# Kernel tuning notes

Measured on AMD Instinct MI355X. Metric: run time of the kernel, lower is better.

Reference implementation:

```python
import jax, jax.numpy as jnp
import numpy as np

B, N, D, H = 4, 512, 4, 256


def _linear_params(key, fan_in, fan_out):
    # torch.nn.Linear default init: U(-1/sqrt(fan_in), 1/sqrt(fan_in))
    lim = 1.0 / np.sqrt(fan_in)
    kw, kb = jax.random.split(key)
    W = jax.random.uniform(kw, (fan_in, fan_out), minval=-lim, maxval=lim, dtype=jnp.float32)
    b = jax.random.uniform(kb, (fan_out,), minval=-lim, maxval=lim, dtype=jnp.float32)
    return W, b


def setup_inputs() -> dict:
    key = jax.random.key(0)
    ks = jax.random.split(key, 8)
    x = jax.random.normal(ks[0], (B, N, D), dtype=jnp.float32)
    adj = jax.random.uniform(ks[1], (B, N, N), dtype=jnp.float32)  # soft adjacency in [0,1)
    W_e1, b_e1 = _linear_params(ks[2], 2 * D, H)
    W_e2, b_e2 = _linear_params(ks[3], H, H)
    W_n1, b_n1 = _linear_params(ks[4], H, H)
    W_n2, b_n2 = _linear_params(ks[5], H, H)
    W_o1, b_o1 = _linear_params(ks[6], D + H, H)
    W_o, b_o = _linear_params(ks[7], H, D)
    return {
        "x": x, "adj": adj,
        "W_e1": W_e1, "b_e1": b_e1, "W_e2": W_e2, "b_e2": b_e2,
        "W_n1": W_n1, "b_n1": b_n1, "W_n2": W_n2, "b_n2": b_n2,
        "W_o1": W_o1, "b_o1": b_o1, "W_o": W_o, "b_o": b_o,
    }


def reference(x, adj, W_e1, b_e1, W_e2, b_e2, W_n1, b_n1, W_n2, b_n2, W_o1, b_o1, W_o, b_o):
    b_, n_, d_ = x.shape
    # innode[b,i,j,:] = x[b,j]; outnode[b,i,j,:] = x[b,i]
    innode = jnp.broadcast_to(x[:, None, :, :], (b_, n_, n_, d_))
    outnode = jnp.broadcast_to(x[:, :, None, :], (b_, n_, n_, d_))
    edge_in = jnp.concatenate([innode, outnode], axis=-1)          # [B,N,N,2D]
    node2edge = jax.nn.relu(edge_in @ W_e1 + b_e1)                 # [B,N,N,H]
    edge2edge = jax.nn.relu(node2edge @ W_e2 + b_e2)               # [B,N,N,H]
    # adjacency-masked sum over axis 1 (the i axis)
    agg = jnp.einsum('bij,bijh->bjh', adj, edge2edge)              # [B,N,H]
    out1 = jax.nn.relu(agg @ W_n1 + b_n1)
    out2 = jax.nn.relu(out1 @ W_n2 + b_n2)
    out3 = jnp.concatenate([x, out2], axis=-1)                     # [B,N,D+H]
    out4 = out3 @ W_o1 + b_o1
    out5 = out4 @ W_o + b_o                                        # [B,N,D]
    # CONTINUOUS is False for the classifier variant
    return jax.nn.log_softmax(out5, axis=2)
```

## Files before the change

### kernel.cpp

```cpp
#include <hip/hip_runtime.h>
#include <hip/hip_fp16.h>
#include <math.h>

#define Bq 4
#define Nq 512
#define Dq 4
#define Hq 256

typedef _Float16 f16x8 __attribute__((ext_vector_type(8)));
typedef float f32x4 __attribute__((ext_vector_type(4)));

__device__ __forceinline__ f16x8 hadd_relu(f16x8 u, f16x8 v) {
    f16x8 s = u + v;
    const f16x8 z = (f16x8)(_Float16)0.0f;
    return __builtin_elementwise_max(s, z);
}

__device__ __forceinline__ uint4 cvt8h(const float* p) {
    union { __half h[8]; uint4 u; } r;
#pragma unroll
    for (int i = 0; i < 8; ++i) r.h[i] = __float2half(p[i]);
    return r.u;
}

__global__ __launch_bounds__(256) void prep_all(
    const float* __restrict__ x, const float* __restrict__ We1,
    const float* __restrict__ be1, __half* __restrict__ U, __half* __restrict__ V,
    const float* __restrict__ Wn1, const float* __restrict__ Wn2,
    const float* __restrict__ Wo1, __half* __restrict__ Wt16) {
    const int bid = blockIdx.x;
    const int t = threadIdx.x;
    if (bid < 256) {
        const float w0 = We1[0 * 256 + t], w1 = We1[1 * 256 + t];
        const float w2 = We1[2 * 256 + t], w3 = We1[3 * 256 + t];
        const float w4 = We1[4 * 256 + t], w5 = We1[5 * 256 + t];
        const float w6 = We1[6 * 256 + t], w7 = We1[7 * 256 + t];
        const float bv = be1[t];
#pragma unroll
        for (int r = 0; r < 8; ++r) {
            const int row = bid * 8 + r;
            const float* xp = x + row * Dq;
            const float x0 = xp[0], x1 = xp[1], x2 = xp[2], x3 = xp[3];
            float u = bv;
            u = fmaf(x0, w0, u); u = fmaf(x1, w1, u);
            u = fmaf(x2, w2, u); u = fmaf(x3, w3, u);
            float v = x0 * w4;
            v = fmaf(x1, w5, v); v = fmaf(x2, w6, v); v = fmaf(x3, w7, v);
            U[(size_t)row * Hq + t] = __float2half(u);
            V[(size_t)row * Hq + t] = __float2half(v);
        }
    } else {
        __shared__ float ld[64][65];
        const int tid = bid - 256;
        const int mat = tid >> 4;
        const int tile = tid & 15;
        const int k0 = (tile >> 2) * 64;
        const int n0 = (tile & 3) * 64;
        const float* W = (mat == 0) ? Wn1 : (mat == 1) ? Wn2 : (Wo1 + 4 * 256);
        const int rr = t >> 6;
        const int cc = t & 63;
#pragma unroll
        for (int r = 0; r < 16; ++r) {
            const int row = r * 4 + rr;
            ld[row][cc] = W[(size_t)(k0 + row) * 256 + n0 + cc];
        }
        __syncthreads();
#pragma unroll
        for (int r = 0; r < 16; ++r) {
            const int nrow = r * 4 + rr;
            Wt16[((size_t)mat * 256 + n0 + nrow) * 256 + k0 + cc] =
                __float2half(ld[cc][nrow]);
        }
    }
}

__global__ __launch_bounds__(256, 2) void edge_gemm(
    const __half* __restrict__ U, const __half* __restrict__ V,
    const float* __restrict__ We2, const float* __restrict__ be2,
    const float* __restrict__ adj, float* __restrict__ aggws) {
    __shared__ __align__(16) char smem[59392];
    __half* Wt = (__half*)smem;
    __half* Us = (__half*)(smem + 32768);
    __half* Vs = (__half*)(smem + 40960);
    float* adjs = (float*)(smem + 57344);
    float* red = (float*)(smem + 40960);

    const int bid = blockIdx.x;
    const int hq_ = bid & 3;
    const int jt = (bid >> 2) & 31;
    const int b = bid >> 7;
    const int h_base = hq_ * 64;
    const int j_base = jt * 16;
    const int t = threadIdx.x;
    const int lane = t & 63;
    const int w = t >> 6;
    const int q = lane >> 4;
    const int l15 = lane & 15;

    const __half* Vb = V + (size_t)b * Nq * Hq;
    const float* adjb = adj + (size_t)b * Nq * Nq;

    const int srow = t >> 4;
    const int sc0 = (t & 15) * 2;

    {
        const int n = t & 63;
        const int swz = n & 31;
        for (int kk = (t >> 6); kk < 256; kk += 4) {
            float val = We2[kk * 256 + h_base + n];
            Wt[n * 256 + ((((kk >> 3) ^ swz)) << 3) + (kk & 7)] = __float2half(val);
        }
    }
    {
        const uint4* gp = (const uint4*)(U + (size_t)(b * Nq + j_base + srow) * Hq);
        uint4 v0 = gp[sc0];
        uint4 v1 = gp[sc0 + 1];
        *(uint4*)&Us[srow * 256 + ((sc0 ^ srow) << 3)] = v0;
        *(uint4*)&Us[srow * 256 + (((sc0 + 1) ^ srow) << 3)] = v1;
    }

    float bias[4];
#pragma unroll
    for (int nt = 0; nt < 4; ++nt) bias[nt] = be2[h_base + nt * 16 + l15];

    f32x4 agg[4];
#pragma unroll
    for (int nt = 0; nt < 4; ++nt) agg[nt] = (f32x4){0.f, 0.f, 0.f, 0.f};

    uint4 pva, pvb; float pad_;
    {
        const uint4* gp = (const uint4*)(Vb + (size_t)(0 + srow) * Hq);
        pva = gp[sc0]; pvb = gp[sc0 + 1];
        pad_ = adjb[(size_t)(0 + srow) * Nq + j_base + (t & 15)];
        *(uint4*)&Vs[0 * 4096 + srow * 256 + ((sc0 ^ srow) << 3)] = pva;
        *(uint4*)&Vs[0 * 4096 + srow * 256 + (((sc0 + 1) ^ srow) << 3)] = pvb;
        adjs[0 * 256 + t] = pad_;
    }
    {
        const uint4* gp = (const uint4*)(Vb + (size_t)(16 + srow) * Hq);
        pva = gp[sc0]; pvb = gp[sc0 + 1];
        pad_ = adjb[(size_t)(16 + srow) * Nq + j_base + (t & 15)];
    }
    __syncthreads();

    const f32x4 zero4 = (f32x4){0.f, 0.f, 0.f, 0.f};

    for (int ch = 0; ch < 32; ++ch) {
        const int cur = ch & 1;
        const __half* Vcur = Vs + cur * 4096;
        const float* Acur = adjs + cur * 256;

        f32x4 acc[4][4];
#pragma unroll
        for (int mi = 0; mi < 4; ++mi)
#pragma unroll
            for (int nt = 0; nt < 4; ++nt)
                acc[mi][nt] = (f32x4){bias[nt], bias[nt], bias[nt], bias[nt]};

#pragma unroll
        for (int ks = 0; ks < 8; ++ks) {
            const int c = ks * 4 + q;
            const f16x8 uvec = *(const f16x8*)&Us[l15 * 256 + ((c ^ l15) << 3)];
            f16x8 afrag[4];
#pragma unroll
            for (int mi = 0; mi < 4; ++mi) {
                const int iv = w * 4 + mi;
                const f16x8 vvec = *(const f16x8*)&Vcur[iv * 256 + ((c ^ iv) << 3)];
                afrag[mi] = hadd_relu(uvec, vvec);
            }
            f16x8 bf[4];
#pragma unroll
            for (int nt = 0; nt < 4; ++nt) {
                const int rn = nt * 16 + l15;
                bf[nt] = *(const f16x8*)&Wt[rn * 256 + ((c ^ (rn & 31)) << 3)];
            }
#pragma unroll
            for (int mi = 0; mi < 4; ++mi)
#pragma unroll
                for (int nt = 0; nt < 4; ++nt)
                    acc[mi][nt] = __builtin_amdgcn_mfma_f32_16x16x32_f16(
                        afrag[mi], bf[nt], acc[mi][nt], 0, 0, 0);
        }

#pragma unroll
        for (int mi = 0; mi < 4; ++mi) {
            const int iv = w * 4 + mi;
            const f32x4 av = *(const f32x4*)&Acur[iv * 16 + q * 4];
#pragma unroll
            for (int nt = 0; nt < 4; ++nt) {
                const f32x4 rel = __builtin_elementwise_max(acc[mi][nt], zero4);
                agg[nt] = av * rel + agg[nt];
            }
        }

        if (ch < 31) {
            const int nxt = cur ^ 1;
            *(uint4*)&Vs[nxt * 4096 + srow * 256 + ((sc0 ^ srow) << 3)] = pva;
            *(uint4*)&Vs[nxt * 4096 + srow * 256 + (((sc0 + 1) ^ srow) << 3)] = pvb;
            adjs[nxt * 256 + t] = pad_;
            if (ch < 30) {
                const int i_base = (ch + 2) * 16;
                const uint4* gp = (const uint4*)(Vb + (size_t)(i_base + srow) * Hq);
                pva = gp[sc0]; pvb = gp[sc0 + 1];
                pad_ = adjb[(size_t)(i_base + srow) * Nq + j_base + (t & 15)];
            }
        }
        __syncthreads();
    }

#pragma unroll
    for (int nt = 0; nt < 4; ++nt)
#pragma unroll
        for (int r = 0; r < 4; ++r)
            red[w * 1024 + (q * 4 + r) * 64 + nt * 16 + l15] = agg[nt][r];
    __syncthreads();
    {
        const int j = t >> 4;
        const int h0 = (t & 15) * 4;
        f32x4 s = *(const f32x4*)&red[0 * 1024 + j * 64 + h0];
        s += *(const f32x4*)&red[1 * 1024 + j * 64 + h0];
        s += *(const f32x4*)&red[2 * 1024 + j * 64 + h0];
        s += *(const f32x4*)&red[3 * 1024 + j * 64 + h0];
        *(f32x4*)&aggws[(size_t)(b * Nq + j_base + j) * Hq + h_base + h0] = s;
    }
}

__global__ __launch_bounds__(256) void tail_kernel(
    const float* __restrict__ aggws, const float* __restrict__ x,
    const __half* __restrict__ Wt16,
    const float* __restrict__ bn1, const float* __restrict__ bn2,
    const float* __restrict__ Wo1, const float* __restrict__ bo1,
    const float* __restrict__ Wo, const float* __restrict__ bo,
    float* __restrict__ out) {
    __shared__ __align__(16) __half actA[16 * 256];
    __shared__ __align__(16) __half actB[16 * 256];
    __shared__ float xs[16][4];
    __shared__ float part[4][16][4];
    __shared__ float s5[16][4];
    const int g0 = blockIdx.x * 16;
    const int t = threadIdx.x;
    const int lane = t & 63;
    const int w = t >> 6;
    const int q = lane >> 4;
    const int l15 = lane & 15;
    const int hb = w * 64;

    {
        const int row = t >> 4;
        const int g = (t & 15) * 2;
        const float* src = aggws + (size_t)(g0 + row) * 256;
        *(uint4*)&actA[row * 256 + ((g ^ row) << 3)] = cvt8h(src + g * 8);
        *(uint4*)&actA[row * 256 + (((g + 1) ^ row) << 3)] = cvt8h(src + g * 8 + 8);
    }
    if (t < 64) xs[t >> 2][t & 3] = x[(size_t)(g0 + (t >> 2)) * 4 + (t & 3)];
    __syncthreads();

    f32x4 acc[4];
#pragma unroll
    for (int nt = 0; nt < 4; ++nt) {
        const float bv = bn1[hb + nt * 16 + l15];
        acc[nt] = (f32x4){bv, bv, bv, bv};
    }
#pragma unroll
    for (int ks = 0; ks < 8; ++ks) {
        const int c = ks * 4 + q;
        const f16x8 af = *(const f16x8*)&actA[l15 * 256 + ((c ^ l15) << 3)];
#pragma unroll
        for (int nt = 0; nt < 4; ++nt) {
            const f16x8 bf = *(const f16x8*)&Wt16[(size_t)(hb + nt * 16 + l15) * 256 + c * 8];
            acc[nt] = __builtin_amdgcn_mfma_f32_16x16x32_f16(af, bf, acc[nt], 0, 0, 0);
        }
    }
#pragma unroll
    for (int nt = 0; nt < 4; ++nt) {
        const int n = hb + nt * 16 + l15;
        const int g = n >> 3;
#pragma unroll
        for (int r = 0; r < 4; ++r) {
            const int row = q * 4 + r;
            actB[row * 256 + ((g ^ row) << 3) + (n & 7)] = __float2half(fmaxf(acc[nt][r], 0.f));
        }
    }
    __syncthreads();

#pragma unroll
    for (int nt = 0; nt < 4; ++nt) {
        const float bv = bn2[hb + nt * 16 + l15];
        acc[nt] = (f32x4){bv, bv, bv, bv};
    }
#pragma unroll
    for (int ks = 0; ks < 8; ++ks) {
        const int c = ks * 4 + q;
        const f16x8 af = *(const f16x8*)&actB[l15 * 256 + ((c ^ l15) << 3)];
#pragma unroll
        for (int nt = 0; nt < 4; ++nt) {
            const f16x8 bf = *(const f16x8*)&Wt16[65536 + (size_t)(hb + nt * 16 + l15) * 256 + c * 8];
            acc[nt] = __builtin_amdgcn_mfma_f32_16x16x32_f16(af, bf, acc[nt], 0, 0, 0);
        }
    }
#pragma unroll
    for (int nt = 0; nt < 4; ++nt) {
        const int n = hb + nt * 16 + l15;
        const int g = n >> 3;
#pragma unroll
        for (int r = 0; r < 4; ++r) {
            const int row = q * 4 + r;
            actA[row * 256 + ((g ^ row) << 3) + (n & 7)] = __float2half(fmaxf(acc[nt][r], 0.f));
        }
    }
    __syncthreads();

#pragma unroll
    for (int nt = 0; nt < 4; ++nt) {
        const int n = hb + nt * 16 + l15;
        const float bv = bo1[n];
        const float w0 = Wo1[0 * 256 + n], w1 = Wo1[1 * 256 + n];
        const float w2 = Wo1[2 * 256 + n], w3 = Wo1[3 * 256 + n];
#pragma unroll
        for (int r = 0; r < 4; ++r) {
            const int row = q * 4 + r;
            float v = bv;
            v = fmaf(xs[row][0], w0, v); v = fmaf(xs[row][1], w1, v);
            v = fmaf(xs[row][2], w2, v); v = fmaf(xs[row][3], w3, v);
            acc[nt][r] = v;
        }
    }
#pragma unroll
    for (int ks = 0; ks < 8; ++ks) {
        const int c = ks * 4 + q;
        const f16x8 af = *(const f16x8*)&actA[l15 * 256 + ((c ^ l15) << 3)];
#pragma unroll
        for (int nt = 0; nt < 4; ++nt) {
            const f16x8 bf = *(const f16x8*)&Wt16[2 * 65536 + (size_t)(hb + nt * 16 + l15) * 256 + c * 8];
            acc[nt] = __builtin_amdgcn_mfma_f32_16x16x32_f16(af, bf, acc[nt], 0, 0, 0);
        }
    }

    float p[4][4];
#pragma unroll
    for (int r = 0; r < 4; ++r)
#pragma unroll
        for (int d = 0; d < 4; ++d) p[r][d] = 0.f;
#pragma unroll
    for (int nt = 0; nt < 4; ++nt) {
        const int n = hb + nt * 16 + l15;
        const float4 wv = *(const float4*)&Wo[n * 4];
#pragma unroll
        for (int r = 0; r < 4; ++r) {
            p[r][0] = fmaf(acc[nt][r], wv.x, p[r][0]);
            p[r][1] = fmaf(acc[nt][r], wv.y, p[r][1]);
            p[r][2] = fmaf(acc[nt][r], wv.z, p[r][2]);
            p[r][3] = fmaf(acc[nt][r], wv.w, p[r][3]);
        }
    }
#pragma unroll
    for (int off = 1; off < 16; off <<= 1)
#pragma unroll
        for (int r = 0; r < 4; ++r)
#pragma unroll
            for (int d = 0; d < 4; ++d)
                p[r][d] += __shfl_xor(p[r][d], off);
    if (l15 == 0) {
#pragma unroll
        for (int r = 0; r < 4; ++r)
#pragma unroll
            for (int d = 0; d < 4; ++d) part[w][q * 4 + r][d] = p[r][d];
    }
    __syncthreads();
    if (t < 64) {
        const int row = t >> 2;
        const int d = t & 3;
        s5[row][d] = part[0][row][d] + part[1][row][d] + part[2][row][d]
                   + part[3][row][d] + bo[d];
    }
    __syncthreads();
    if (t < 16) {
        const float v0 = s5[t][0], v1 = s5[t][1], v2 = s5[t][2], v3 = s5[t][3];
        const float m = fmaxf(fmaxf(v0, v1), fmaxf(v2, v3));
        const float s = expf(v0 - m) + expf(v1 - m) + expf(v2 - m) + expf(v3 - m);
        const float lse = m + logf(s);
        float* op = out + (size_t)(g0 + t) * 4;
        op[0] = v0 - lse; op[1] = v1 - lse; op[2] = v2 - lse; op[3] = v3 - lse;
    }
}

extern "C" void kernel_launch(void* const* d_in, const int* in_sizes, int n_in,
                              void* d_out, int out_size, void* d_ws, size_t ws_size,
                              hipStream_t stream) {
    const float* x   = (const float*)d_in[0];
    const float* adj = (const float*)d_in[1];
    const float* We1 = (const float*)d_in[2];
    const float* be1 = (const float*)d_in[3];
    const float* We2 = (const float*)d_in[4];
    const float* be2 = (const float*)d_in[5];
    const float* Wn1 = (const float*)d_in[6];
    const float* bn1 = (const float*)d_in[7];
    const float* Wn2 = (const float*)d_in[8];
    const float* bn2 = (const float*)d_in[9];
    const float* Wo1 = (const float*)d_in[10];
    const float* bo1 = (const float*)d_in[11];
    const float* Wo  = (const float*)d_in[12];
    const float* bo  = (const float*)d_in[13];
    float* out = (float*)d_out;

    __half* U = (__half*)d_ws;
    __half* V = U + (size_t)Bq * Nq * Hq;
    float* aggws = (float*)((char*)d_ws + (size_t)2 * Bq * Nq * Hq * sizeof(__half));
    __half* Wt16 = (__half*)((char*)d_ws + (size_t)4 * 1024 * 1024);

    prep_all<<<304, 256, 0, stream>>>(x, We1, be1, U, V, Wn1, Wn2, Wo1, Wt16);
    edge_gemm<<<512, 256, 0, stream>>>(U, V, We2, be2, adj, aggws);
    tail_kernel<<<128, 256, 0, stream>>>(aggws, x, Wt16, bn1, bn2, Wo1, bo1, Wo, bo, out);
}
```

Before: 227.3 us.

## Quad-buffer V/adj tiles to halve barriers and raise MFMA wave priority

Grows the shared V and adjacency staging from two buffers to four and processes two 16-row chunks per loop iteration. This halves the number of __syncthreads and gives the register prefetches two chunks of lead time. It also wraps the MFMA loop in s_setprio so matrix work is prioritised over other waves. Shared memory per block rises to about 76 KB, which may limit how many blocks fit per CU alongside the launch bound of 2, and the extra prefetch registers add register pressure.

```diff
diff --git a/kernel.cpp b/kernel.cpp
--- a/kernel.cpp
+++ b/kernel.cpp
@@ -78,11 +78,11 @@
     const __half* __restrict__ U, const __half* __restrict__ V,
     const float* __restrict__ We2, const float* __restrict__ be2,
     const float* __restrict__ adj, float* __restrict__ aggws) {
-    __shared__ __align__(16) char smem[59392];
+    __shared__ __align__(16) char smem[77824];
     __half* Wt = (__half*)smem;
     __half* Us = (__half*)(smem + 32768);
     __half* Vs = (__half*)(smem + 40960);
-    float* adjs = (float*)(smem + 57344);
+    float* adjs = (float*)(smem + 73728);
     float* red = (float*)(smem + 40960);
 
     const int bid = blockIdx.x;
@@ -127,29 +127,40 @@
 #pragma unroll
     for (int nt = 0; nt < 4; ++nt) agg[nt] = (f32x4){0.f, 0.f, 0.f, 0.f};
 
-    uint4 pva, pvb; float pad_;
-    {
-        const uint4* gp = (const uint4*)(Vb + (size_t)(0 + srow) * Hq);
-        pva = gp[sc0]; pvb = gp[sc0 + 1];
-        pad_ = adjb[(size_t)(0 + srow) * Nq + j_base + (t & 15)];
-        *(uint4*)&Vs[0 * 4096 + srow * 256 + ((sc0 ^ srow) << 3)] = pva;
-        *(uint4*)&Vs[0 * 4096 + srow * 256 + (((sc0 + 1) ^ srow) << 3)] = pvb;
-        adjs[0 * 256 + t] = pad_;
+    const f32x4 zero4 = (f32x4){0.f, 0.f, 0.f, 0.f};
+
+    uint4 pvaA, pvbA; float padA;
+    uint4 pvaB, pvbB; float padB;
+
+    {
+        const uint4* gp = (const uint4*)(Vb + (size_t)srow * Hq);
+        pvaA = gp[sc0]; pvbA = gp[sc0 + 1];
+        padA = adjb[(size_t)srow * Nq + j_base + (t & 15)];
+        *(uint4*)&Vs[0 * 4096 + srow * 256 + ((sc0 ^ srow) << 3)] = pvaA;
+        *(uint4*)&Vs[0 * 4096 + srow * 256 + (((sc0 + 1) ^ srow) << 3)] = pvbA;
+        adjs[0 * 256 + t] = padA;
     }
     {
         const uint4* gp = (const uint4*)(Vb + (size_t)(16 + srow) * Hq);
-        pva = gp[sc0]; pvb = gp[sc0 + 1];
-        pad_ = adjb[(size_t)(16 + srow) * Nq + j_base + (t & 15)];
-    }
-    __syncthreads();
-
-    const f32x4 zero4 = (f32x4){0.f, 0.f, 0.f, 0.f};
-
-    for (int ch = 0; ch < 32; ++ch) {
-        const int cur = ch & 1;
-        const __half* Vcur = Vs + cur * 4096;
-        const float* Acur = adjs + cur * 256;
-
+        pvaB = gp[sc0]; pvbB = gp[sc0 + 1];
+        padB = adjb[(size_t)(16 + srow) * Nq + j_base + (t & 15)];
+        *(uint4*)&Vs[1 * 4096 + srow * 256 + ((sc0 ^ srow) << 3)] = pvaB;
+        *(uint4*)&Vs[1 * 4096 + srow * 256 + (((sc0 + 1) ^ srow) << 3)] = pvbB;
+        adjs[1 * 256 + t] = padB;
+    }
+    {
+        const uint4* gp = (const uint4*)(Vb + (size_t)(32 + srow) * Hq);
+        pvaA = gp[sc0]; pvbA = gp[sc0 + 1];
+        padA = adjb[(size_t)(32 + srow) * Nq + j_base + (t & 15)];
+    }
+    {
+        const uint4* gp = (const uint4*)(Vb + (size_t)(48 + srow) * Hq);
+        pvaB = gp[sc0]; pvbB = gp[sc0 + 1];
+        padB = adjb[(size_t)(48 + srow) * Nq + j_base + (t & 15)];
+    }
+    __syncthreads();
+
+    auto compute_chunk = [&](const __half* Vcur, const float* Acur) {
         f32x4 acc[4][4];
 #pragma unroll
         for (int mi = 0; mi < 4; ++mi)
@@ -157,6 +168,7 @@
             for (int nt = 0; nt < 4; ++nt)
                 acc[mi][nt] = (f32x4){bias[nt], bias[nt], bias[nt], bias[nt]};
 
+        __builtin_amdgcn_s_setprio(1);
 #pragma unroll
         for (int ks = 0; ks < 8; ++ks) {
             const int c = ks * 4 + q;
@@ -181,6 +193,7 @@
                     acc[mi][nt] = __builtin_amdgcn_mfma_f32_16x16x32_f16(
                         afrag[mi], bf[nt], acc[mi][nt], 0, 0, 0);
         }
+        __builtin_amdgcn_s_setprio(0);
 
 #pragma unroll
         for (int mi = 0; mi < 4; ++mi) {
@@ -192,17 +205,35 @@
                 agg[nt] = av * rel + agg[nt];
             }
         }
-
-        if (ch < 31) {
-            const int nxt = cur ^ 1;
-            *(uint4*)&Vs[nxt * 4096 + srow * 256 + ((sc0 ^ srow) << 3)] = pva;
-            *(uint4*)&Vs[nxt * 4096 + srow * 256 + (((sc0 + 1) ^ srow) << 3)] = pvb;
-            adjs[nxt * 256 + t] = pad_;
-            if (ch < 30) {
-                const int i_base = (ch + 2) * 16;
+    };
+
+    for (int pair = 0; pair < 16; ++pair) {
+        const int cur = (pair & 1) * 2;
+        const int nxt = ((pair + 1) & 1) * 2;
+
+        compute_chunk(Vs + cur * 4096, adjs + cur * 256);
+        if (pair < 15) {
+            *(uint4*)&Vs[nxt * 4096 + srow * 256 + ((sc0 ^ srow) << 3)] = pvaA;
+            *(uint4*)&Vs[nxt * 4096 + srow * 256 + (((sc0 + 1) ^ srow) << 3)] = pvbA;
+            adjs[nxt * 256 + t] = padA;
+            if (pair < 14) {
+                const int i_base = (2 * pair + 4) * 16;
                 const uint4* gp = (const uint4*)(Vb + (size_t)(i_base + srow) * Hq);
-                pva = gp[sc0]; pvb = gp[sc0 + 1];
-                pad_ = adjb[(size_t)(i_base + srow) * Nq + j_base + (t & 15)];
+                pvaA = gp[sc0]; pvbA = gp[sc0 + 1];
+                padA = adjb[(size_t)(i_base + srow) * Nq + j_base + (t & 15)];
+            }
+        }
+
+        compute_chunk(Vs + (cur + 1) * 4096, adjs + (cur + 1) * 256);
+        if (pair < 15) {
+            *(uint4*)&Vs[(nxt + 1) * 4096 + srow * 256 + ((sc0 ^ srow) << 3)] = pvaB;
+            *(uint4*)&Vs[(nxt + 1) * 4096 + srow * 256 + (((sc0 + 1) ^ srow) << 3)] = pvbB;
+            adjs[(nxt + 1) * 256 + t] = padB;
+            if (pair < 14) {
+                const int i_base = (2 * pair + 5) * 16;
+                const uint4* gp = (const uint4*)(Vb + (size_t)(i_base + srow) * Hq);
+                pvaB = gp[sc0]; pvbB = gp[sc0 + 1];
+                padB = adjb[(size_t)(i_base + srow) * Nq + j_base + (t & 15)];
             }
         }
         __syncthreads();
```

Result: slower. 323.5 us (+42.3%).
